# Performance work log

Measured on AMD Instinct MI355X. Metric: run time of the kernel, lower is better.

The kernel has to match this reference:

```python
import jax, jax.numpy as jnp
import numpy as np

B = 65536  # batch size


def setup_inputs() -> dict:
    key = jax.random.key(0)
    kx, kw, kb = jax.random.split(key, 3)
    x = jax.random.normal(kx, (B, 784), dtype=jnp.float32)
    W = jax.random.normal(kw, (10, 784), dtype=jnp.float32) * 0.03
    b = jax.random.normal(kb, (10,), dtype=jnp.float32) * 0.03
    return {"x": x, "W": W, "b": b}


def _quanv_features(x):
    # x: [B, 784] -> [B, 28, 28] -> 2x2 patches in row-major patch order,
    # each patch flattened as [p(r,c), p(r,c+1), p(r+1,c), p(r+1,c+1)].
    Bn = x.shape[0]
    p = x.reshape(Bn, 14, 2, 14, 2).transpose(0, 1, 3, 2, 4).reshape(Bn, 196, 4)
    # Analytic 4-qubit circuit: RY(x_i)|0>, CNOT(0,1), CNOT(2,3), <Z_i>
    # => [cos x0, cos x0 * cos x1, cos x2, cos x2 * cos x3]
    c = jnp.cos(p)
    m = jnp.stack(
        [c[..., 0], c[..., 0] * c[..., 1], c[..., 2], c[..., 2] * c[..., 3]],
        axis=-1,
    )
    # residual add with the raw patch, then concat over 196 patches -> [B, 784]
    return (m + p).reshape(Bn, 784)


def reference(x, W, b):
    feats = _quanv_features(x)              # [B, 784]
    logits = feats @ W.T + b                # [B, 10]
    return jax.nn.log_softmax(logits, axis=-1)
```

## Files before the change

### kernel.cpp

```cpp
#include <hip/hip_runtime.h>
#include <hip/hip_bf16.h>
#include <stdint.h>


typedef __attribute__((ext_vector_type(8))) short short8;
typedef __attribute__((ext_vector_type(4))) float f32x4;

__global__ void quanv_wprep_kernel(const float* __restrict__ Wm,
                                   uint32_t* __restrict__ ws) {
    const int idx = blockIdx.x * 256 + threadIdx.x;
    if (idx >= 6400) return;
    const int kt  = idx >> 8;
    const int rem = idx & 255;
    const int l   = rem >> 2;
    const int d   = rem & 3;
    const int n   = l & 15;
    const int kg  = l >> 4;
    uint32_t outv = 0;
    if (n < 10) {
        uint32_t hv[2];
#pragma unroll
        for (int d2 = 0; d2 < 2; ++d2) {
            const int e  = 2 * d + d2;
            const int jp = 32 * kt + 4 * kg + 16 * (e >> 2) + 2 * ((e >> 1) & 1);
            float v = 0.f;
            if (jp < 784) {
                const int ri = jp / 28;
                const int pc = (jp % 28) >> 1;
                const int pr = ri >> 1;
                const int ho = ri & 1;
                const int col = (pr * 14 + pc) * 4 + 2 * ho + (e & 1);
                v = Wm[n * 784 + col];
            }
            hv[d2] = (uint32_t)__bfloat16_as_ushort(__float2bfloat16(v));
        }
        outv = hv[0] | (hv[1] << 16);
    }
    ws[idx] = outv;
}

#define FEAT8(VA, VB, A) do {                                                 \
    { const float ce=__cosf((VA).x), co=__cosf((VA).y);                       \
      (A)[0]=(short)__bfloat16_as_ushort(__float2bfloat16(ce + (VA).x));      \
      (A)[1]=(short)__bfloat16_as_ushort(__float2bfloat16(fmaf(ce,co,(VA).y)));}\
    { const float ce=__cosf((VA).z), co=__cosf((VA).w);                       \
      (A)[2]=(short)__bfloat16_as_ushort(__float2bfloat16(ce + (VA).z));      \
      (A)[3]=(short)__bfloat16_as_ushort(__float2bfloat16(fmaf(ce,co,(VA).w)));}\
    { const float ce=__cosf((VB).x), co=__cosf((VB).y);                       \
      (A)[4]=(short)__bfloat16_as_ushort(__float2bfloat16(ce + (VB).x));      \
      (A)[5]=(short)__bfloat16_as_ushort(__float2bfloat16(fmaf(ce,co,(VB).y)));}\
    { const float ce=__cosf((VB).z), co=__cosf((VB).w);                       \
      (A)[6]=(short)__bfloat16_as_ushort(__float2bfloat16(ce + (VB).z));      \
      (A)[7]=(short)__bfloat16_as_ushort(__float2bfloat16(fmaf(ce,co,(VB).w)));}\
} while (0)

#define QKB(KT, WF) do {                                                      \
    const float4 va = *(const float4*)(px + 32 * (KT));                       \
    const float4 vb = *(const float4*)(px + 32 * (KT) + 16);                  \
    short8 a; FEAT8(va, vb, a);                                               \
    acc = __builtin_amdgcn_mfma_f32_16x16x32_bf16(a, (WF), acc, 0, 0, 0);     \
} while (0)

__global__ __launch_bounds__(256, 4)
void quanv_mfma5_kernel(const float* __restrict__ x,
                        const char* __restrict__ wsb,
                        const float* __restrict__ bias,
                        float* __restrict__ out) {
    __shared__ f32x4 red[2][64];

    const int t   = threadIdx.x;
    const int l   = t & 63;
    const int w   = t >> 6;
    const int rg  = __builtin_amdgcn_readfirstlane(w >> 1);
    const int kh  = __builtin_amdgcn_readfirstlane(w & 1);
    const int r16 = l & 15;
    const int kg  = l >> 4;
    const int rowBase = blockIdx.x * 32 + rg * 16;
    const float* px = x + (size_t)(rowBase + r16) * 784 + 4 * kg;

    f32x4 acc = {0.f, 0.f, 0.f, 0.f};

    if (kh == 0) {
        const char* wbp = wsb + l * 16;
        const short8 wf0  = *(const short8*)(wbp + 0  * 1024);
        const short8 wf1  = *(const short8*)(wbp + 1  * 1024);
        const short8 wf2  = *(const short8*)(wbp + 2  * 1024);
        const short8 wf3  = *(const short8*)(wbp + 3  * 1024);
        const short8 wf4  = *(const short8*)(wbp + 4  * 1024);
        const short8 wf5  = *(const short8*)(wbp + 5  * 1024);
        const short8 wf6  = *(const short8*)(wbp + 6  * 1024);
        const short8 wf7  = *(const short8*)(wbp + 7  * 1024);
        const short8 wf8  = *(const short8*)(wbp + 8  * 1024);
        const short8 wf9  = *(const short8*)(wbp + 9  * 1024);
        const short8 wf10 = *(const short8*)(wbp + 10 * 1024);
        const short8 wf11 = *(const short8*)(wbp + 11 * 1024);
        const short8 wf12 = *(const short8*)(wbp + 12 * 1024);
        QKB(0, wf0);  QKB(1, wf1);  QKB(2, wf2);  QKB(3, wf3);
        QKB(4, wf4);  QKB(5, wf5);  QKB(6, wf6);  QKB(7, wf7);
        QKB(8, wf8);  QKB(9, wf9);  QKB(10, wf10); QKB(11, wf11);
        QKB(12, wf12);
    } else {
        const char* wbp = wsb + 13 * 1024 + l * 16;
        const short8 wf0  = *(const short8*)(wbp + 0  * 1024);
        const short8 wf1  = *(const short8*)(wbp + 1  * 1024);
        const short8 wf2  = *(const short8*)(wbp + 2  * 1024);
        const short8 wf3  = *(const short8*)(wbp + 3  * 1024);
        const short8 wf4  = *(const short8*)(wbp + 4  * 1024);
        const short8 wf5  = *(const short8*)(wbp + 5  * 1024);
        const short8 wf6  = *(const short8*)(wbp + 6  * 1024);
        const short8 wf7  = *(const short8*)(wbp + 7  * 1024);
        const short8 wf8  = *(const short8*)(wbp + 8  * 1024);
        const short8 wf9  = *(const short8*)(wbp + 9  * 1024);
        const short8 wf10 = *(const short8*)(wbp + 10 * 1024);
        const short8 wf11 = *(const short8*)(wbp + 11 * 1024);
        QKB(13, wf0);  QKB(14, wf1);  QKB(15, wf2);  QKB(16, wf3);
        QKB(17, wf4);  QKB(18, wf5);  QKB(19, wf6);  QKB(20, wf7);
        QKB(21, wf8);  QKB(22, wf9);  QKB(23, wf10);
        {
            const float4 va = *(const float4*)(px + 32 * 24);
            const float4 vb = *(const float4*)(px);
            short8 a; FEAT8(va, vb, a);
            acc = __builtin_amdgcn_mfma_f32_16x16x32_bf16(a, wf11, acc, 0, 0, 0);
        }
    }

    if (kh == 1) red[rg][l] = acc;
    __syncthreads();
    if (kh == 0) {
        const f32x4 o = red[rg][l];
#pragma unroll
        for (int j = 0; j < 4; ++j) acc[j] += o[j];

        const float bn = bias[r16 < 10 ? r16 : 0];
#pragma unroll
        for (int j = 0; j < 4; ++j) {
            float v = (r16 < 10) ? (acc[j] + bn) : -1e30f;
            float mx = v;
            mx = fmaxf(mx, __shfl_xor(mx, 1, 64));
            mx = fmaxf(mx, __shfl_xor(mx, 2, 64));
            mx = fmaxf(mx, __shfl_xor(mx, 4, 64));
            mx = fmaxf(mx, __shfl_xor(mx, 8, 64));
            float e = (r16 < 10) ? __expf(v - mx) : 0.f;
            float s = e;
            s += __shfl_xor(s, 1, 64);
            s += __shfl_xor(s, 2, 64);
            s += __shfl_xor(s, 4, 64);
            s += __shfl_xor(s, 8, 64);
            const float ls = __logf(s) + mx;
            if (r16 < 10)
                out[(size_t)(rowBase + 4 * kg + j) * 10 + r16] = v - ls;
        }
    }
}

extern "C" void kernel_launch(void* const* d_in, const int* in_sizes, int n_in,
                              void* d_out, int out_size, void* d_ws, size_t ws_size,
                              hipStream_t stream) {
    const float* x    = (const float*)d_in[0];
    const float* Wm   = (const float*)d_in[1];
    const float* bias = (const float*)d_in[2];
    float* out        = (float*)d_out;

    quanv_wprep_kernel<<<dim3(25), dim3(256), 0, stream>>>(
        Wm, (uint32_t*)d_ws);
    quanv_mfma5_kernel<<<dim3(2048), dim3(256), 0, stream>>>(
        x, (const char*)d_ws, bias, out);
}
```

Before: 42.68 us.

## Split K across four waves per 16-row tile and batch all loads upfront

Each block now handles 16 rows with four waves each covering about a quarter of the K tiles, instead of 32 rows with two waves per row group. Each wave first issues all of its x and weight loads, then does the cosine features and MFMAs, so more memory requests are in flight at once. The grid doubles to 4096 blocks and the shared-memory reduction now sums three partial accumulators. The cost is more reduction traffic and more registers held by the batched loads.

New measurement: 40.00 us. 1.07x faster.

```diff
diff --git a/kernel.cpp b/kernel.cpp
--- a/kernel.cpp
+++ b/kernel.cpp
@@ -54,82 +54,60 @@
       (A)[7]=(short)__bfloat16_as_ushort(__float2bfloat16(fmaf(ce,co,(VB).w)));}\
 } while (0)
 
-#define QKB(KT, WF) do {                                                      \
-    const float4 va = *(const float4*)(px + 32 * (KT));                       \
-    const float4 vb = *(const float4*)(px + 32 * (KT) + 16);                  \
-    short8 a; FEAT8(va, vb, a);                                               \
-    acc = __builtin_amdgcn_mfma_f32_16x16x32_bf16(a, (WF), acc, 0, 0, 0);     \
-} while (0)
+template <int KT0, int N>
+__device__ __forceinline__ void quarter(const float* __restrict__ px,
+                                        const char* __restrict__ wsb,
+                                        int l, f32x4& acc) {
+    float4 va[N], vb[N];
+    short8 wf[N];
+    const char* wbp = wsb + KT0 * 1024 + l * 16;
+#pragma unroll
+    for (int j = 0; j < N; ++j) {
+        const int kt = KT0 + j;
+        va[j] = *(const float4*)(px + 32 * kt);
+        vb[j] = (kt == 24) ? *(const float4*)(px)
+                           : *(const float4*)(px + 32 * kt + 16);
+        wf[j] = *(const short8*)(wbp + j * 1024);
+    }
+#pragma unroll
+    for (int j = 0; j < N; ++j) {
+        short8 a;
+        FEAT8(va[j], vb[j], a);
+        acc = __builtin_amdgcn_mfma_f32_16x16x32_bf16(a, wf[j], acc, 0, 0, 0);
+    }
+}
 
 __global__ __launch_bounds__(256, 4)
-void quanv_mfma5_kernel(const float* __restrict__ x,
+void quanv_mfma6_kernel(const float* __restrict__ x,
                         const char* __restrict__ wsb,
                         const float* __restrict__ bias,
                         float* __restrict__ out) {
-    __shared__ f32x4 red[2][64];
+    __shared__ f32x4 red[3][64];
 
     const int t   = threadIdx.x;
     const int l   = t & 63;
-    const int w   = t >> 6;
-    const int rg  = __builtin_amdgcn_readfirstlane(w >> 1);
-    const int kh  = __builtin_amdgcn_readfirstlane(w & 1);
+    const int kq  = __builtin_amdgcn_readfirstlane(t >> 6);
     const int r16 = l & 15;
     const int kg  = l >> 4;
-    const int rowBase = blockIdx.x * 32 + rg * 16;
+    const int rowBase = blockIdx.x * 16;
     const float* px = x + (size_t)(rowBase + r16) * 784 + 4 * kg;
 
     f32x4 acc = {0.f, 0.f, 0.f, 0.f};
 
-    if (kh == 0) {
-        const char* wbp = wsb + l * 16;
-        const short8 wf0  = *(const short8*)(wbp + 0  * 1024);
-        const short8 wf1  = *(const short8*)(wbp + 1  * 1024);
-        const short8 wf2  = *(const short8*)(wbp + 2  * 1024);
-        const short8 wf3  = *(const short8*)(wbp + 3  * 1024);
-        const short8 wf4  = *(const short8*)(wbp + 4  * 1024);
-        const short8 wf5  = *(const short8*)(wbp + 5  * 1024);
-        const short8 wf6  = *(const short8*)(wbp + 6  * 1024);
-        const short8 wf7  = *(const short8*)(wbp + 7  * 1024);
-        const short8 wf8  = *(const short8*)(wbp + 8  * 1024);
-        const short8 wf9  = *(const short8*)(wbp + 9  * 1024);
-        const short8 wf10 = *(const short8*)(wbp + 10 * 1024);
-        const short8 wf11 = *(const short8*)(wbp + 11 * 1024);
-        const short8 wf12 = *(const short8*)(wbp + 12 * 1024);
-        QKB(0, wf0);  QKB(1, wf1);  QKB(2, wf2);  QKB(3, wf3);
-        QKB(4, wf4);  QKB(5, wf5);  QKB(6, wf6);  QKB(7, wf7);
-        QKB(8, wf8);  QKB(9, wf9);  QKB(10, wf10); QKB(11, wf11);
-        QKB(12, wf12);
-    } else {
-        const char* wbp = wsb + 13 * 1024 + l * 16;
-        const short8 wf0  = *(const short8*)(wbp + 0  * 1024);
-        const short8 wf1  = *(const short8*)(wbp + 1  * 1024);
-        const short8 wf2  = *(const short8*)(wbp + 2  * 1024);
-        const short8 wf3  = *(const short8*)(wbp + 3  * 1024);
-        const short8 wf4  = *(const short8*)(wbp + 4  * 1024);
-        const short8 wf5  = *(const short8*)(wbp + 5  * 1024);
-        const short8 wf6  = *(const short8*)(wbp + 6  * 1024);
-        const short8 wf7  = *(const short8*)(wbp + 7  * 1024);
-        const short8 wf8  = *(const short8*)(wbp + 8  * 1024);
-        const short8 wf9  = *(const short8*)(wbp + 9  * 1024);
-        const short8 wf10 = *(const short8*)(wbp + 10 * 1024);
-        const short8 wf11 = *(const short8*)(wbp + 11 * 1024);
-        QKB(13, wf0);  QKB(14, wf1);  QKB(15, wf2);  QKB(16, wf3);
-        QKB(17, wf4);  QKB(18, wf5);  QKB(19, wf6);  QKB(20, wf7);
-        QKB(21, wf8);  QKB(22, wf9);  QKB(23, wf10);
-        {
-            const float4 va = *(const float4*)(px + 32 * 24);
-            const float4 vb = *(const float4*)(px);
-            short8 a; FEAT8(va, vb, a);
-            acc = __builtin_amdgcn_mfma_f32_16x16x32_bf16(a, wf11, acc, 0, 0, 0);
+    if      (kq == 0) quarter<0, 7>(px, wsb, l, acc);
+    else if (kq == 1) quarter<7, 6>(px, wsb, l, acc);
+    else if (kq == 2) quarter<13, 6>(px, wsb, l, acc);
+    else              quarter<19, 6>(px, wsb, l, acc);
+
+    if (kq != 0) red[kq - 1][l] = acc;
+    __syncthreads();
+    if (kq == 0) {
+#pragma unroll
+        for (int s = 0; s < 3; ++s) {
+            const f32x4 o = red[s][l];
+#pragma unroll
+            for (int j = 0; j < 4; ++j) acc[j] += o[j];
         }
-    }
-
-    if (kh == 1) red[rg][l] = acc;
-    __syncthreads();
-    if (kh == 0) {
-        const f32x4 o = red[rg][l];
-#pragma unroll
-        for (int j = 0; j < 4; ++j) acc[j] += o[j];
 
         const float bn = bias[r16 < 10 ? r16 : 0];
 #pragma unroll
@@ -163,6 +141,6 @@
 
     quanv_wprep_kernel<<<dim3(25), dim3(256), 0, stream>>>(
         Wm, (uint32_t*)d_ws);
-    quanv_mfma5_kernel<<<dim3(2048), dim3(256), 0, stream>>>(
+    quanv_mfma6_kernel<<<dim3(4096), dim3(256), 0, stream>>>(
         x, (const char*)d_ws, bias, out);
 }
```
